# Kernel tuning notes

Hardware: AMD Instinct MI355X
Metric: run time of the kernel (lower is better)

The kernel has to match this reference:

```python
import jax, jax.numpy as jnp
import numpy as np

N_NODES = 100000
N_EDGES = 1600000
F_IN = 128
HIDDEN = 64
N_CLASSES = 32


def setup_inputs() -> dict:
    key = jax.random.key(0)
    k1, k2, k3, k4 = jax.random.split(key, 4)
    x = jax.random.normal(k1, (N_NODES, F_IN), dtype=jnp.float32)
    edge_index = jax.random.randint(k2, (2, N_EDGES), 0, N_NODES, dtype=jnp.int32)
    # Glorot-style init for the two GCNConv weight matrices
    W1 = jax.random.normal(k3, (F_IN, HIDDEN), dtype=jnp.float32) * (1.0 / np.sqrt(F_IN))
    W2 = jax.random.normal(k4, (HIDDEN, N_CLASSES), dtype=jnp.float32) * (1.0 / np.sqrt(HIDDEN))
    b1 = jnp.zeros((HIDDEN,), dtype=jnp.float32)
    b2 = jnp.zeros((N_CLASSES,), dtype=jnp.float32)
    return {"x": x, "edge_index": edge_index, "W1": W1, "b1": b1, "W2": W2, "b2": b2}


def gcn_conv(x, W, b, src, dst, num_nodes):
    # PyG GCNConv: linear transform first, then normalized neighbor aggregation.
    h = x @ W  # [N, out]
    ones = jnp.ones(src.shape, dtype=h.dtype)
    deg = jax.ops.segment_sum(ones, dst, num_segments=num_nodes)  # in-degree incl. self-loops
    d_inv_sqrt = jnp.where(deg > 0, jax.lax.rsqrt(deg), 0.0)
    norm = d_inv_sqrt[src] * d_inv_sqrt[dst]  # [E]
    msg = h[src] * norm[:, None]              # gather + scale, [E, out]
    out = jax.ops.segment_sum(msg, dst, num_segments=num_nodes)  # scatter-add
    return out + b


def reference(x, edge_index, W1, b1, W2, b2):
    n = x.shape[0]
    # add_self_loops=True (GCNConv default)
    loop = jnp.arange(n, dtype=edge_index.dtype)
    src = jnp.concatenate([edge_index[0], loop])
    dst = jnp.concatenate([edge_index[1], loop])
    h = jax.nn.relu(gcn_conv(x, W1, b1, src, dst, n))
    # F.dropout(training=self.training) is identity in eval mode
    logits = gcn_conv(h, W2, b2, src, dst, n)
    return jax.nn.log_softmax(logits, axis=1)
```

## Files before the change

### kernel.cpp

```cpp
#include <hip/hip_runtime.h>

#define F_IN 128
#define HID 64
#define CLS 32
#define BCAP 8192

typedef short v8s __attribute__((ext_vector_type(8)));
typedef float f4 __attribute__((ext_vector_type(4)));
typedef float f2 __attribute__((ext_vector_type(2)));

__device__ __forceinline__ float bflo(unsigned int w) { return __uint_as_float(w << 16); }
__device__ __forceinline__ float bfhi(unsigned int w) { return __uint_as_float(w & 0xFFFF0000u); }
__device__ __forceinline__ unsigned short f2bf(float f) {
    unsigned int u = __float_as_uint(f);
    u += 0x7FFFu + ((u >> 16) & 1u);
    return (unsigned short)(u >> 16);
}
__device__ __forceinline__ unsigned int pack2(float lo, float hi) {
    return (unsigned int)f2bf(lo) | ((unsigned int)f2bf(hi) << 16);
}
__device__ __forceinline__ unsigned char f2fp8(float v) {
    return (unsigned char)(__builtin_amdgcn_cvt_pk_fp8_f32(v, v, 0, false) & 0xFF);
}

__global__ __launch_bounds__(512) void k_init(int* __restrict__ bCursor, int nb) {
    int i = threadIdx.x;
    if (i < nb) bCursor[i] = i * BCAP;
}

__global__ __launch_bounds__(256) void k_bscatter(const int* __restrict__ src,
                                                  const int* __restrict__ dst,
                                                  int* __restrict__ bCursor,
                                                  int* __restrict__ bucketed, int E, int nb) {
    __shared__ int h[512];
    __shared__ int chunk[512];
    int tid = threadIdx.x;
    for (int i = tid; i < nb; i += 256) h[i] = 0;
    __syncthreads();

    int e0 = blockIdx.x * 2048;
    int myRec[8], myB[8], myRank[8];
#pragma unroll
    for (int k = 0; k < 8; ++k) {
        int e = e0 + k * 256 + tid;
        if (e < E) {
            int d = dst[e];
            myB[k] = d >> 8;
            myRec[k] = src[e] | ((d & 255) << 17);
            myRank[k] = atomicAdd(&h[myB[k]], 1);
        } else {
            myB[k] = -1;
        }
    }
    __syncthreads();
    for (int i = tid; i < nb; i += 256)
        chunk[i] = h[i] ? atomicAdd(&bCursor[i], h[i]) : 0;
    __syncthreads();
#pragma unroll
    for (int k = 0; k < 8; ++k) {
        if (myB[k] >= 0) bucketed[chunk[myB[k]] + myRank[k]] = myRec[k];
    }
}

__global__ __launch_bounds__(512) void k_csr(const int* __restrict__ bCursor,
                                             const int* __restrict__ bucketed,
                                             int* __restrict__ pk,
                                             float* __restrict__ dinv, int* __restrict__ csr,
                                             int n) {
    __shared__ int cnt[256];
    __shared__ int s[256];
    __shared__ int baseS[256];
    int b = blockIdx.x;
    int node0 = b << 8;
    int tid = threadIdx.x;
    if (tid < 256) cnt[tid] = 0;
    __syncthreads();
    int p0 = b * BCAP, p1 = bCursor[b];

    int rec[16], rnk[16];
#pragma unroll
    for (int k = 0; k < 16; ++k) {
        int p = p0 + tid + (k << 9);
        if (p < p1) {
            int r = bucketed[p];
            rec[k] = r;
            rnk[k] = atomicAdd(&cnt[r >> 17], 1);
        } else {
            rec[k] = -1;
        }
    }
    __syncthreads();
    int v = 0;
    if (tid < 256) { v = cnt[tid]; s[tid] = v; }
    __syncthreads();
    for (int off = 1; off < 256; off <<= 1) {
        int t = (tid >= off && tid < 256) ? s[tid - off] : 0;
        __syncthreads();
        if (tid < 256) s[tid] += t;
        __syncthreads();
    }
    if (tid < 256) {
        int myoff = p0 + s[tid] - v;
        baseS[tid] = myoff;
        int node = node0 + tid;
        if (node < n) {
            pk[node] = myoff | (v << 22);
            dinv[node] = rsqrtf((float)(v + 1));
        }
    }
    __syncthreads();
#pragma unroll
    for (int k = 0; k < 16; ++k) {
        if (rec[k] >= 0) csr[baseS[rec[k] >> 17] + rnk[k]] = rec[k] & 0x1FFFF;
    }
}

__global__ __launch_bounds__(256) void k_gemm1(const float* __restrict__ x,
                                               const float* __restrict__ W,
                                               const float* __restrict__ dinv,
                                               unsigned char* __restrict__ y, int n) {
    __shared__ unsigned short Wt[HID * 136];
    int tid = threadIdx.x;
    for (int i = tid; i < F_IN * HID; i += 256) {
        int k = i >> 6, nn = i & 63;
        Wt[nn * 136 + k] = f2bf(W[i]);
    }
    __syncthreads();

    int lane = tid & 63;
    int quad = lane >> 4, c = lane & 15;
    int nstripes = (n + 15) >> 4;
    int stripe = blockIdx.x * 4 + (tid >> 6);
    if (stripe >= nstripes) return;
    int row0 = stripe << 4;

    f4 acc[4] = {};
    union { unsigned int u[4]; v8s v; } au;

#pragma unroll
    for (int ks = 0; ks < 4; ++ks) {
        int k0 = ks * 32 + quad * 8;
        int row = row0 + c;
        if (row >= n) row = n - 1;
        const float* xp = x + (size_t)row * F_IN + k0;
        float4 lo = *(const float4*)xp;
        float4 hi = *(const float4*)(xp + 4);
        au.u[0] = pack2(lo.x, lo.y);
        au.u[1] = pack2(lo.z, lo.w);
        au.u[2] = pack2(hi.x, hi.y);
        au.u[3] = pack2(hi.z, hi.w);
        v8s a = au.v;
#pragma unroll
        for (int nt = 0; nt < 4; ++nt) {
            v8s bb = *(const v8s*)&Wt[(nt * 16 + c) * 136 + k0];
            acc[nt] = __builtin_amdgcn_mfma_f32_16x16x32_bf16(a, bb, acc[nt], 0, 0, 0);
        }
    }

#pragma unroll
    for (int reg = 0; reg < 4; ++reg) {
        int row = row0 + quad * 4 + reg;
        if (row < n) {
            float dd = dinv[row];
#pragma unroll
            for (int nt = 0; nt < 4; ++nt)
                y[(size_t)row * HID + nt * 16 + c] = f2fp8(acc[nt][reg] * dd);
        }
    }
}

__global__ __launch_bounds__(256) void k_gather64_w2(const int* __restrict__ pk,
                                                     const int* __restrict__ csr,
                                                     const unsigned char* __restrict__ xw8,
                                                     const float* __restrict__ b1,
                                                     const float* __restrict__ W2,
                                                     const float* __restrict__ dinv,
                                                     unsigned short* __restrict__ y2, int n) {
    __shared__ unsigned short Wt[CLS * 72];
    __shared__ unsigned short Hl[32 * 72];
    int tid = threadIdx.x;
    for (int i = tid; i < HID * CLS; i += 256) {
        int k = i >> 5, nn = i & 31;
        Wt[nn * 72 + k] = f2bf(W2[i]);
    }

    int g = tid >> 3;
    int l = tid & 7;
    int node = blockIdx.x * 32 + g;
    bool alive = node < n;

    if (alive) {
        unsigned int pv = (unsigned int)pk[node];
        int p0 = pv & 0x3FFFFF;
        int cntv = (int)(pv >> 22);
        int p1 = p0 + cntv;
        float dd = rsqrtf((float)(cntv + 1));
        uint2 sw = *(const uint2*)(xw8 + (size_t)node * HID + l * 8);

        f2 a0 = {0.f, 0.f}, a1 = a0, a2 = a0, a3 = a0;
        f2 c0 = a0, c1 = a0, c2 = a0, c3 = a0;
        int p = p0;
        for (; p + 3 < p1; p += 4) {
            int s0 = csr[p], s1 = csr[p + 1], s2 = csr[p + 2], s3 = csr[p + 3];
            uint2 w0 = *(const uint2*)(xw8 + (size_t)s0 * HID + l * 8);
            uint2 w1 = *(const uint2*)(xw8 + (size_t)s1 * HID + l * 8);
            uint2 w2 = *(const uint2*)(xw8 + (size_t)s2 * HID + l * 8);
            uint2 w3 = *(const uint2*)(xw8 + (size_t)s3 * HID + l * 8);
            a0 += __builtin_amdgcn_cvt_pk_f32_fp8(w0.x, false);
            a1 += __builtin_amdgcn_cvt_pk_f32_fp8(w0.x, true);
            a2 += __builtin_amdgcn_cvt_pk_f32_fp8(w0.y, false);
            a3 += __builtin_amdgcn_cvt_pk_f32_fp8(w0.y, true);
            c0 += __builtin_amdgcn_cvt_pk_f32_fp8(w1.x, false);
            c1 += __builtin_amdgcn_cvt_pk_f32_fp8(w1.x, true);
            c2 += __builtin_amdgcn_cvt_pk_f32_fp8(w1.y, false);
            c3 += __builtin_amdgcn_cvt_pk_f32_fp8(w1.y, true);
            a0 += __builtin_amdgcn_cvt_pk_f32_fp8(w2.x, false);
            a1 += __builtin_amdgcn_cvt_pk_f32_fp8(w2.x, true);
            a2 += __builtin_amdgcn_cvt_pk_f32_fp8(w2.y, false);
            a3 += __builtin_amdgcn_cvt_pk_f32_fp8(w2.y, true);
            c0 += __builtin_amdgcn_cvt_pk_f32_fp8(w3.x, false);
            c1 += __builtin_amdgcn_cvt_pk_f32_fp8(w3.x, true);
            c2 += __builtin_amdgcn_cvt_pk_f32_fp8(w3.y, false);
            c3 += __builtin_amdgcn_cvt_pk_f32_fp8(w3.y, true);
        }
        for (; p < p1; ++p) {
            int s0 = csr[p];
            uint2 w0 = *(const uint2*)(xw8 + (size_t)s0 * HID + l * 8);
            a0 += __builtin_amdgcn_cvt_pk_f32_fp8(w0.x, false);
            a1 += __builtin_amdgcn_cvt_pk_f32_fp8(w0.x, true);
            a2 += __builtin_amdgcn_cvt_pk_f32_fp8(w0.y, false);
            a3 += __builtin_amdgcn_cvt_pk_f32_fp8(w0.y, true);
        }
        a0 += c0; a1 += c1; a2 += c2; a3 += c3;
        a0 += __builtin_amdgcn_cvt_pk_f32_fp8(sw.x, false);
        a1 += __builtin_amdgcn_cvt_pk_f32_fp8(sw.x, true);
        a2 += __builtin_amdgcn_cvt_pk_f32_fp8(sw.y, false);
        a3 += __builtin_amdgcn_cvt_pk_f32_fp8(sw.y, true);

        float4 bb0 = *(const float4*)(b1 + l * 8);
        float4 bb1 = *(const float4*)(b1 + l * 8 + 4);
        float h0 = fmaxf(a0.x * dd + bb0.x, 0.f);
        float h1 = fmaxf(a0.y * dd + bb0.y, 0.f);
        float h2 = fmaxf(a1.x * dd + bb0.z, 0.f);
        float h3 = fmaxf(a1.y * dd + bb0.w, 0.f);
        float h4 = fmaxf(a2.x * dd + bb1.x, 0.f);
        float h5 = fmaxf(a2.y * dd + bb1.y, 0.f);
        float h6 = fmaxf(a3.x * dd + bb1.z, 0.f);
        float h7 = fmaxf(a3.y * dd + bb1.w, 0.f);
        uint4 hp;
        hp.x = pack2(h0, h1);
        hp.y = pack2(h2, h3);
        hp.z = pack2(h4, h5);
        hp.w = pack2(h6, h7);
        *(uint4*)&Hl[g * 72 + l * 8] = hp;
    }
    __syncthreads();

    int wv = tid >> 6;
    int t = wv & 1, nt = wv >> 1;
    int lane = tid & 63, quad = lane >> 4, c = lane & 15;
    f4 acc = {};
#pragma unroll
    for (int ks = 0; ks < 2; ++ks) {
        int k0 = ks * 32 + quad * 8;
        v8s aF = *(const v8s*)&Hl[(t * 16 + c) * 72 + k0];
        v8s bF = *(const v8s*)&Wt[(nt * 16 + c) * 72 + k0];
        acc = __builtin_amdgcn_mfma_f32_16x16x32_bf16(aF, bF, acc, 0, 0, 0);
    }
    int row0 = blockIdx.x * 32 + t * 16;
#pragma unroll
    for (int reg = 0; reg < 4; ++reg) {
        int row = row0 + quad * 4 + reg;
        if (row < n) {
            float dd2 = dinv[row];
            y2[(size_t)row * CLS + nt * 16 + c] = f2bf(acc[reg] * dd2);
        }
    }
}

__global__ __launch_bounds__(256) void k_gather32_lsm(const int* __restrict__ pk,
                                                      const int* __restrict__ csr,
                                                      const unsigned short* __restrict__ hwb,
                                                      const float* __restrict__ b,
                                                      float* __restrict__ out, int n) {
    int tid = threadIdx.x;
    int node = blockIdx.x * 64 + (tid >> 2);
    if (node >= n) return;
    int l = tid & 3;
    unsigned int pv = (unsigned int)pk[node];
    int p0 = pv & 0x3FFFFF;
    int cntv = (int)(pv >> 22);
    int p1 = p0 + cntv;
    float dd = rsqrtf((float)(cntv + 1));
    uint4 sw = *(const uint4*)(hwb + (size_t)node * CLS + l * 8);

    float A0 = 0.f, A1 = 0.f, A2 = 0.f, A3 = 0.f, A4 = 0.f, A5 = 0.f, A6 = 0.f, A7 = 0.f;
    float B0 = 0.f, B1 = 0.f, B2 = 0.f, B3 = 0.f, B4 = 0.f, B5 = 0.f, B6 = 0.f, B7 = 0.f;
    int p = p0;
    for (; p + 3 < p1; p += 4) {
        int s0 = csr[p], s1 = csr[p + 1], s2 = csr[p + 2], s3 = csr[p + 3];
        uint4 w0 = *(const uint4*)(hwb + (size_t)s0 * CLS + l * 8);
        uint4 w1 = *(const uint4*)(hwb + (size_t)s1 * CLS + l * 8);
        uint4 w2 = *(const uint4*)(hwb + (size_t)s2 * CLS + l * 8);
        uint4 w3 = *(const uint4*)(hwb + (size_t)s3 * CLS + l * 8);
        A0 += bflo(w0.x); A1 += bfhi(w0.x); A2 += bflo(w0.y); A3 += bfhi(w0.y);
        A4 += bflo(w0.z); A5 += bfhi(w0.z); A6 += bflo(w0.w); A7 += bfhi(w0.w);
        B0 += bflo(w1.x); B1 += bfhi(w1.x); B2 += bflo(w1.y); B3 += bfhi(w1.y);
        B4 += bflo(w1.z); B5 += bfhi(w1.z); B6 += bflo(w1.w); B7 += bfhi(w1.w);
        A0 += bflo(w2.x); A1 += bfhi(w2.x); A2 += bflo(w2.y); A3 += bfhi(w2.y);
        A4 += bflo(w2.z); A5 += bfhi(w2.z); A6 += bflo(w2.w); A7 += bfhi(w2.w);
        B0 += bflo(w3.x); B1 += bfhi(w3.x); B2 += bflo(w3.y); B3 += bfhi(w3.y);
        B4 += bflo(w3.z); B5 += bfhi(w3.z); B6 += bflo(w3.w); B7 += bfhi(w3.w);
    }
    for (; p < p1; ++p) {
        int s0 = csr[p];
        uint4 w0 = *(const uint4*)(hwb + (size_t)s0 * CLS + l * 8);
        A0 += bflo(w0.x); A1 += bfhi(w0.x); A2 += bflo(w0.y); A3 += bfhi(w0.y);
        A4 += bflo(w0.z); A5 += bfhi(w0.z); A6 += bflo(w0.w); A7 += bfhi(w0.w);
    }
    A0 += B0; A1 += B1; A2 += B2; A3 += B3;
    A4 += B4; A5 += B5; A6 += B6; A7 += B7;

    float4 bb0 = *(const float4*)(b + l * 8);
    float4 bb1 = *(const float4*)(b + l * 8 + 4);
    float v0 = (A0 + bflo(sw.x)) * dd + bb0.x;
    float v1 = (A1 + bfhi(sw.x)) * dd + bb0.y;
    float v2 = (A2 + bflo(sw.y)) * dd + bb0.z;
    float v3 = (A3 + bfhi(sw.y)) * dd + bb0.w;
    float v4 = (A4 + bflo(sw.z)) * dd + bb1.x;
    float v5 = (A5 + bfhi(sw.z)) * dd + bb1.y;
    float v6 = (A6 + bflo(sw.w)) * dd + bb1.z;
    float v7 = (A7 + bfhi(sw.w)) * dd + bb1.w;

    float m = fmaxf(fmaxf(fmaxf(v0, v1), fmaxf(v2, v3)), fmaxf(fmaxf(v4, v5), fmaxf(v6, v7)));
    m = fmaxf(m, __shfl_xor(m, 1));
    m = fmaxf(m, __shfl_xor(m, 2));
    float s = __expf(v0 - m) + __expf(v1 - m) + __expf(v2 - m) + __expf(v3 - m) +
              __expf(v4 - m) + __expf(v5 - m) + __expf(v6 - m) + __expf(v7 - m);
    s += __shfl_xor(s, 1);
    s += __shfl_xor(s, 2);
    float ls = m + __logf(s);
    float4 o0, o1;
    o0.x = v0 - ls; o0.y = v1 - ls; o0.z = v2 - ls; o0.w = v3 - ls;
    o1.x = v4 - ls; o1.y = v5 - ls; o1.z = v6 - ls; o1.w = v7 - ls;
    float* op = out + (size_t)node * CLS + l * 8;
    *(float4*)op = o0;
    *(float4*)(op + 4) = o1;
}

extern "C" void kernel_launch(void* const* d_in, const int* in_sizes, int n_in,
                              void* d_out, int out_size, void* d_ws, size_t ws_size,
                              hipStream_t stream) {
    const float* x  = (const float*)d_in[0];
    const int* edge = (const int*)d_in[1];
    const float* W1 = (const float*)d_in[2];
    const float* b1 = (const float*)d_in[3];
    const float* W2 = (const float*)d_in[4];
    const float* b2 = (const float*)d_in[5];
    float* out = (float*)d_out;

    int N = in_sizes[0] / F_IN;
    int E = in_sizes[1] / 2;
    const int* src = edge;
    const int* dst = edge + E;
    int NB = (N + 255) >> 8;

    float* dinv    = (float*)d_ws;
    int* pk        = (int*)(dinv + N);
    int* bCursor   = pk + N;
    int* csr       = bCursor + 512;
    int* bucketed  = csr + (size_t)NB * BCAP;
    unsigned char* bufA = (unsigned char*)(bucketed + (size_t)NB * BCAP);
    unsigned short* y2  = (unsigned short*)(bufA + (size_t)N * HID);

    k_init<<<1, 512, 0, stream>>>(bCursor, NB);
    k_bscatter<<<(E + 2047) / 2048, 256, 0, stream>>>(src, dst, bCursor, bucketed, E, NB);
    k_csr<<<NB, 512, 0, stream>>>(bCursor, bucketed, pk, dinv, csr, N);

    int nstripes16 = (N + 15) >> 4;
    int gemmBlocks = (nstripes16 + 3) / 4;

    k_gemm1<<<gemmBlocks, 256, 0, stream>>>(x, W1, dinv, bufA, N);

    k_gather64_w2<<<(N + 31) / 32, 256, 0, stream>>>(pk, csr, bufA, b1, W2, dinv, y2, N);

    k_gather32_lsm<<<(N + 63) / 64, 256, 0, stream>>>(pk, csr, y2, b2, out, N);
}
```

Before: 203.0 us.

## Fuse all GCN stages into one cooperative persistent kernel with grid syncs

Replaces the six separate launches with a single cooperative kernel. Inside it, part of the grid does the edge bucketing while the rest pulls GEMM1 jobs from an atomic work queue, so the two stages overlap. Grid-wide syncs then separate the CSR build, the layer-1 gather with the W2 transform, and the layer-2 gather with log-softmax. GEMM1 no longer depends on dinv: its output is stored unscaled and the source-side dinv is applied per neighbour during the gather. This adds an extra dinv load per edge, and grid.sync overhead plus the lower per-CU occupancy cap can offset the saved launches. The bf16 packing also switches to the v_cvt_pk_bf16_f32 instruction.

```diff
diff --git a/kernel.cpp b/kernel.cpp
--- a/kernel.cpp
+++ b/kernel.cpp
@@ -1,4 +1,7 @@
 #include <hip/hip_runtime.h>
+#include <hip/hip_cooperative_groups.h>
+
+namespace cg = cooperative_groups;
 
 #define F_IN 128
 #define HID 64
@@ -17,335 +20,324 @@
     return (unsigned short)(u >> 16);
 }
 __device__ __forceinline__ unsigned int pack2(float lo, float hi) {
-    return (unsigned int)f2bf(lo) | ((unsigned int)f2bf(hi) << 16);
+    unsigned int r;
+    asm("v_cvt_pk_bf16_f32 %0, %1, %2" : "=v"(r) : "v"(lo), "v"(hi));
+    return r;
 }
 __device__ __forceinline__ unsigned char f2fp8(float v) {
     return (unsigned char)(__builtin_amdgcn_cvt_pk_fp8_f32(v, v, 0, false) & 0xFF);
 }
 
-__global__ __launch_bounds__(512) void k_init(int* __restrict__ bCursor, int nb) {
-    int i = threadIdx.x;
-    if (i < nb) bCursor[i] = i * BCAP;
-}
-
-__global__ __launch_bounds__(256) void k_bscatter(const int* __restrict__ src,
-                                                  const int* __restrict__ dst,
-                                                  int* __restrict__ bCursor,
-                                                  int* __restrict__ bucketed, int E, int nb) {
-    __shared__ int h[512];
-    __shared__ int chunk[512];
-    int tid = threadIdx.x;
-    for (int i = tid; i < nb; i += 256) h[i] = 0;
-    __syncthreads();
-
-    int e0 = blockIdx.x * 2048;
-    int myRec[8], myB[8], myRank[8];
-#pragma unroll
-    for (int k = 0; k < 8; ++k) {
-        int e = e0 + k * 256 + tid;
-        if (e < E) {
-            int d = dst[e];
-            myB[k] = d >> 8;
-            myRec[k] = src[e] | ((d & 255) << 17);
-            myRank[k] = atomicAdd(&h[myB[k]], 1);
-        } else {
-            myB[k] = -1;
-        }
-    }
-    __syncthreads();
-    for (int i = tid; i < nb; i += 256)
-        chunk[i] = h[i] ? atomicAdd(&bCursor[i], h[i]) : 0;
-    __syncthreads();
-#pragma unroll
-    for (int k = 0; k < 8; ++k) {
-        if (myB[k] >= 0) bucketed[chunk[myB[k]] + myRank[k]] = myRec[k];
-    }
-}
-
-__global__ __launch_bounds__(512) void k_csr(const int* __restrict__ bCursor,
-                                             const int* __restrict__ bucketed,
-                                             int* __restrict__ pk,
-                                             float* __restrict__ dinv, int* __restrict__ csr,
-                                             int n) {
-    __shared__ int cnt[256];
-    __shared__ int s[256];
-    __shared__ int baseS[256];
-    int b = blockIdx.x;
-    int node0 = b << 8;
-    int tid = threadIdx.x;
-    if (tid < 256) cnt[tid] = 0;
-    __syncthreads();
-    int p0 = b * BCAP, p1 = bCursor[b];
-
-    int rec[16], rnk[16];
-#pragma unroll
-    for (int k = 0; k < 16; ++k) {
-        int p = p0 + tid + (k << 9);
-        if (p < p1) {
-            int r = bucketed[p];
-            rec[k] = r;
-            rnk[k] = atomicAdd(&cnt[r >> 17], 1);
-        } else {
-            rec[k] = -1;
-        }
-    }
-    __syncthreads();
-    int v = 0;
-    if (tid < 256) { v = cnt[tid]; s[tid] = v; }
-    __syncthreads();
-    for (int off = 1; off < 256; off <<= 1) {
-        int t = (tid >= off && tid < 256) ? s[tid - off] : 0;
-        __syncthreads();
-        if (tid < 256) s[tid] += t;
-        __syncthreads();
-    }
-    if (tid < 256) {
-        int myoff = p0 + s[tid] - v;
-        baseS[tid] = myoff;
-        int node = node0 + tid;
-        if (node < n) {
-            pk[node] = myoff | (v << 22);
-            dinv[node] = rsqrtf((float)(v + 1));
-        }
-    }
-    __syncthreads();
-#pragma unroll
-    for (int k = 0; k < 16; ++k) {
-        if (rec[k] >= 0) csr[baseS[rec[k] >> 17] + rnk[k]] = rec[k] & 0x1FFFF;
-    }
-}
-
-__global__ __launch_bounds__(256) void k_gemm1(const float* __restrict__ x,
-                                               const float* __restrict__ W,
-                                               const float* __restrict__ dinv,
-                                               unsigned char* __restrict__ y, int n) {
-    __shared__ unsigned short Wt[HID * 136];
-    int tid = threadIdx.x;
-    for (int i = tid; i < F_IN * HID; i += 256) {
-        int k = i >> 6, nn = i & 63;
-        Wt[nn * 136 + k] = f2bf(W[i]);
-    }
-    __syncthreads();
-
-    int lane = tid & 63;
-    int quad = lane >> 4, c = lane & 15;
-    int nstripes = (n + 15) >> 4;
-    int stripe = blockIdx.x * 4 + (tid >> 6);
-    if (stripe >= nstripes) return;
-    int row0 = stripe << 4;
-
-    f4 acc[4] = {};
-    union { unsigned int u[4]; v8s v; } au;
-
-#pragma unroll
-    for (int ks = 0; ks < 4; ++ks) {
-        int k0 = ks * 32 + quad * 8;
-        int row = row0 + c;
-        if (row >= n) row = n - 1;
-        const float* xp = x + (size_t)row * F_IN + k0;
-        float4 lo = *(const float4*)xp;
-        float4 hi = *(const float4*)(xp + 4);
-        au.u[0] = pack2(lo.x, lo.y);
-        au.u[1] = pack2(lo.z, lo.w);
-        au.u[2] = pack2(hi.x, hi.y);
-        au.u[3] = pack2(hi.z, hi.w);
-        v8s a = au.v;
-#pragma unroll
-        for (int nt = 0; nt < 4; ++nt) {
-            v8s bb = *(const v8s*)&Wt[(nt * 16 + c) * 136 + k0];
-            acc[nt] = __builtin_amdgcn_mfma_f32_16x16x32_bf16(a, bb, acc[nt], 0, 0, 0);
-        }
-    }
-
-#pragma unroll
-    for (int reg = 0; reg < 4; ++reg) {
-        int row = row0 + quad * 4 + reg;
-        if (row < n) {
-            float dd = dinv[row];
-#pragma unroll
-            for (int nt = 0; nt < 4; ++nt)
-                y[(size_t)row * HID + nt * 16 + c] = f2fp8(acc[nt][reg] * dd);
-        }
-    }
-}
-
-__global__ __launch_bounds__(256) void k_gather64_w2(const int* __restrict__ pk,
-                                                     const int* __restrict__ csr,
-                                                     const unsigned char* __restrict__ xw8,
-                                                     const float* __restrict__ b1,
-                                                     const float* __restrict__ W2,
-                                                     const float* __restrict__ dinv,
-                                                     unsigned short* __restrict__ y2, int n) {
-    __shared__ unsigned short Wt[CLS * 72];
-    __shared__ unsigned short Hl[32 * 72];
-    int tid = threadIdx.x;
+struct GP {
+    const float* x; const int* src; const int* dst;
+    const float* W1; const float* b1; const float* W2; const float* b2;
+    float* out;
+    float* dinv; int* pk; int* bC; int* qctr; int* csr; int* bucketed;
+    unsigned char* bufA; unsigned short* y2;
+    int N, E, NB, split;
+};
+
+union SU {
+    struct { int h[512]; int chunk[512]; } sc;
+    struct { int cnt[256]; int s[256]; int cur[256]; } cs;
+    unsigned short w1[HID * 136];
+    struct { unsigned short Wt[CLS * 72]; unsigned short Hl[32 * 72]; } g;
+};
+
+__global__ __launch_bounds__(256, 4) void k_fused(GP p) {
+    __shared__ SU S;
+    __shared__ int jslot;
+    cg::grid_group grid = cg::this_grid();
+    const int tid = threadIdx.x;
+    const int bid = blockIdx.x;
+    const int GD = gridDim.x;
+    const int lane = tid & 63;
+
+    if (bid < p.split) {
+        int nchunks = (p.E + 2047) >> 11;
+        for (int ch = bid; ch < nchunks; ch += p.split) {
+            __syncthreads();
+            for (int i = tid; i < p.NB; i += 256) S.sc.h[i] = 0;
+            __syncthreads();
+            int e0 = ch << 11;
+            int myRec[8], myB[8], myRank[8];
+#pragma unroll
+            for (int k = 0; k < 8; ++k) {
+                int e = e0 + k * 256 + tid;
+                if (e < p.E) {
+                    int d = p.dst[e];
+                    myB[k] = d >> 8;
+                    myRec[k] = p.src[e] | ((d & 255) << 17);
+                    myRank[k] = atomicAdd(&S.sc.h[myB[k]], 1);
+                } else {
+                    myB[k] = -1;
+                }
+            }
+            __syncthreads();
+            for (int i = tid; i < p.NB; i += 256)
+                S.sc.chunk[i] = S.sc.h[i] ? (i * BCAP + atomicAdd(&p.bC[i], S.sc.h[i])) : 0;
+            __syncthreads();
+#pragma unroll
+            for (int k = 0; k < 8; ++k)
+                if (myB[k] >= 0) p.bucketed[S.sc.chunk[myB[k]] + myRank[k]] = myRec[k];
+        }
+        __syncthreads();
+    }
+    {
+        for (int i = tid; i < F_IN * HID; i += 256) {
+            int k = i >> 6, nn = i & 63;
+            S.w1[nn * 136 + k] = f2bf(p.W1[i]);
+        }
+        int nstripes = (p.N + 15) >> 4;
+        int jobs = (nstripes + 3) >> 2;
+        int quad = lane >> 4, c = lane & 15;
+        while (true) {
+            __syncthreads();
+            if (tid == 0) jslot = atomicAdd(p.qctr, 1);
+            __syncthreads();
+            int job = jslot;
+            if (job >= jobs) break;
+            int stripe = job * 4 + (tid >> 6);
+            if (stripe < nstripes) {
+                int row0 = stripe << 4;
+                f4 acc[4] = {};
+                union { unsigned int u[4]; v8s v; } au;
+#pragma unroll
+                for (int ks = 0; ks < 4; ++ks) {
+                    int k0 = ks * 32 + quad * 8;
+                    int row = row0 + c;
+                    if (row >= p.N) row = p.N - 1;
+                    const float* xp = p.x + (size_t)row * F_IN + k0;
+                    float4 lo = *(const float4*)xp;
+                    float4 hi = *(const float4*)(xp + 4);
+                    au.u[0] = pack2(lo.x, lo.y);
+                    au.u[1] = pack2(lo.z, lo.w);
+                    au.u[2] = pack2(hi.x, hi.y);
+                    au.u[3] = pack2(hi.z, hi.w);
+                    v8s a = au.v;
+#pragma unroll
+                    for (int nt = 0; nt < 4; ++nt) {
+                        v8s bb = *(const v8s*)&S.w1[(nt * 16 + c) * 136 + k0];
+                        acc[nt] = __builtin_amdgcn_mfma_f32_16x16x32_bf16(a, bb, acc[nt], 0, 0, 0);
+                    }
+                }
+#pragma unroll
+                for (int reg = 0; reg < 4; ++reg) {
+                    int row = row0 + quad * 4 + reg;
+                    if (row < p.N) {
+#pragma unroll
+                        for (int nt = 0; nt < 4; ++nt)
+                            p.bufA[(size_t)row * HID + nt * 16 + c] = f2fp8(acc[nt][reg]);
+                    }
+                }
+            }
+        }
+    }
+    grid.sync();
+
+    for (int b = bid; b < p.NB; b += GD) {
+        __syncthreads();
+        S.cs.cnt[tid] = 0;
+        __syncthreads();
+        int p0 = b * BCAP, p1 = p0 + p.bC[b];
+        for (int q = p0 + tid; q < p1; q += 256) atomicAdd(&S.cs.cnt[p.bucketed[q] >> 17], 1);
+        __syncthreads();
+        int v = S.cs.cnt[tid];
+        S.cs.s[tid] = v;
+        __syncthreads();
+        for (int off = 1; off < 256; off <<= 1) {
+            int t = (tid >= off) ? S.cs.s[tid - off] : 0;
+            __syncthreads();
+            S.cs.s[tid] += t;
+            __syncthreads();
+        }
+        int myoff = p0 + S.cs.s[tid] - v;
+        S.cs.cur[tid] = myoff;
+        int node = (b << 8) + tid;
+        if (node < p.N) {
+            p.pk[node] = myoff | (v << 22);
+            p.dinv[node] = rsqrtf((float)(v + 1));
+        }
+        __syncthreads();
+        for (int q = p0 + tid; q < p1; q += 256) {
+            int r = p.bucketed[q];
+            int w = atomicAdd(&S.cs.cur[r >> 17], 1);
+            p.csr[w] = r & 0x1FFFF;
+        }
+    }
+    grid.sync();
+
     for (int i = tid; i < HID * CLS; i += 256) {
         int k = i >> 5, nn = i & 31;
-        Wt[nn * 72 + k] = f2bf(W2[i]);
-    }
-
-    int g = tid >> 3;
-    int l = tid & 7;
-    int node = blockIdx.x * 32 + g;
-    bool alive = node < n;
-
-    if (alive) {
-        unsigned int pv = (unsigned int)pk[node];
-        int p0 = pv & 0x3FFFFF;
-        int cntv = (int)(pv >> 22);
-        int p1 = p0 + cntv;
-        float dd = rsqrtf((float)(cntv + 1));
-        uint2 sw = *(const uint2*)(xw8 + (size_t)node * HID + l * 8);
-
-        f2 a0 = {0.f, 0.f}, a1 = a0, a2 = a0, a3 = a0;
-        f2 c0 = a0, c1 = a0, c2 = a0, c3 = a0;
-        int p = p0;
-        for (; p + 3 < p1; p += 4) {
-            int s0 = csr[p], s1 = csr[p + 1], s2 = csr[p + 2], s3 = csr[p + 3];
-            uint2 w0 = *(const uint2*)(xw8 + (size_t)s0 * HID + l * 8);
-            uint2 w1 = *(const uint2*)(xw8 + (size_t)s1 * HID + l * 8);
-            uint2 w2 = *(const uint2*)(xw8 + (size_t)s2 * HID + l * 8);
-            uint2 w3 = *(const uint2*)(xw8 + (size_t)s3 * HID + l * 8);
-            a0 += __builtin_amdgcn_cvt_pk_f32_fp8(w0.x, false);
-            a1 += __builtin_amdgcn_cvt_pk_f32_fp8(w0.x, true);
-            a2 += __builtin_amdgcn_cvt_pk_f32_fp8(w0.y, false);
-            a3 += __builtin_amdgcn_cvt_pk_f32_fp8(w0.y, true);
-            c0 += __builtin_amdgcn_cvt_pk_f32_fp8(w1.x, false);
-            c1 += __builtin_amdgcn_cvt_pk_f32_fp8(w1.x, true);
-            c2 += __builtin_amdgcn_cvt_pk_f32_fp8(w1.y, false);
-            c3 += __builtin_amdgcn_cvt_pk_f32_fp8(w1.y, true);
-            a0 += __builtin_amdgcn_cvt_pk_f32_fp8(w2.x, false);
-            a1 += __builtin_amdgcn_cvt_pk_f32_fp8(w2.x, true);
-            a2 += __builtin_amdgcn_cvt_pk_f32_fp8(w2.y, false);
-            a3 += __builtin_amdgcn_cvt_pk_f32_fp8(w2.y, true);
-            c0 += __builtin_amdgcn_cvt_pk_f32_fp8(w3.x, false);
-            c1 += __builtin_amdgcn_cvt_pk_f32_fp8(w3.x, true);
-            c2 += __builtin_amdgcn_cvt_pk_f32_fp8(w3.y, false);
-            c3 += __builtin_amdgcn_cvt_pk_f32_fp8(w3.y, true);
-        }
-        for (; p < p1; ++p) {
-            int s0 = csr[p];
-            uint2 w0 = *(const uint2*)(xw8 + (size_t)s0 * HID + l * 8);
-            a0 += __builtin_amdgcn_cvt_pk_f32_fp8(w0.x, false);
-            a1 += __builtin_amdgcn_cvt_pk_f32_fp8(w0.x, true);
-            a2 += __builtin_amdgcn_cvt_pk_f32_fp8(w0.y, false);
-            a3 += __builtin_amdgcn_cvt_pk_f32_fp8(w0.y, true);
-        }
-        a0 += c0; a1 += c1; a2 += c2; a3 += c3;
-        a0 += __builtin_amdgcn_cvt_pk_f32_fp8(sw.x, false);
-        a1 += __builtin_amdgcn_cvt_pk_f32_fp8(sw.x, true);
-        a2 += __builtin_amdgcn_cvt_pk_f32_fp8(sw.y, false);
-        a3 += __builtin_amdgcn_cvt_pk_f32_fp8(sw.y, true);
-
-        float4 bb0 = *(const float4*)(b1 + l * 8);
-        float4 bb1 = *(const float4*)(b1 + l * 8 + 4);
-        float h0 = fmaxf(a0.x * dd + bb0.x, 0.f);
-        float h1 = fmaxf(a0.y * dd + bb0.y, 0.f);
-        float h2 = fmaxf(a1.x * dd + bb0.z, 0.f);
-        float h3 = fmaxf(a1.y * dd + bb0.w, 0.f);
-        float h4 = fmaxf(a2.x * dd + bb1.x, 0.f);
-        float h5 = fmaxf(a2.y * dd + bb1.y, 0.f);
-        float h6 = fmaxf(a3.x * dd + bb1.z, 0.f);
-        float h7 = fmaxf(a3.y * dd + bb1.w, 0.f);
-        uint4 hp;
-        hp.x = pack2(h0, h1);
-        hp.y = pack2(h2, h3);
-        hp.z = pack2(h4, h5);
-        hp.w = pack2(h6, h7);
-        *(uint4*)&Hl[g * 72 + l * 8] = hp;
-    }
-    __syncthreads();
-
-    int wv = tid >> 6;
-    int t = wv & 1, nt = wv >> 1;
-    int lane = tid & 63, quad = lane >> 4, c = lane & 15;
-    f4 acc = {};
-#pragma unroll
-    for (int ks = 0; ks < 2; ++ks) {
-        int k0 = ks * 32 + quad * 8;
-        v8s aF = *(const v8s*)&Hl[(t * 16 + c) * 72 + k0];
-        v8s bF = *(const v8s*)&Wt[(nt * 16 + c) * 72 + k0];
-        acc = __builtin_amdgcn_mfma_f32_16x16x32_bf16(aF, bF, acc, 0, 0, 0);
-    }
-    int row0 = blockIdx.x * 32 + t * 16;
-#pragma unroll
-    for (int reg = 0; reg < 4; ++reg) {
-        int row = row0 + quad * 4 + reg;
-        if (row < n) {
-            float dd2 = dinv[row];
-            y2[(size_t)row * CLS + nt * 16 + c] = f2bf(acc[reg] * dd2);
-        }
-    }
-}
-
-__global__ __launch_bounds__(256) void k_gather32_lsm(const int* __restrict__ pk,
-                                                      const int* __restrict__ csr,
-                                                      const unsigned short* __restrict__ hwb,
-                                                      const float* __restrict__ b,
-                                                      float* __restrict__ out, int n) {
-    int tid = threadIdx.x;
-    int node = blockIdx.x * 64 + (tid >> 2);
-    if (node >= n) return;
-    int l = tid & 3;
-    unsigned int pv = (unsigned int)pk[node];
-    int p0 = pv & 0x3FFFFF;
-    int cntv = (int)(pv >> 22);
-    int p1 = p0 + cntv;
-    float dd = rsqrtf((float)(cntv + 1));
-    uint4 sw = *(const uint4*)(hwb + (size_t)node * CLS + l * 8);
-
-    float A0 = 0.f, A1 = 0.f, A2 = 0.f, A3 = 0.f, A4 = 0.f, A5 = 0.f, A6 = 0.f, A7 = 0.f;
-    float B0 = 0.f, B1 = 0.f, B2 = 0.f, B3 = 0.f, B4 = 0.f, B5 = 0.f, B6 = 0.f, B7 = 0.f;
-    int p = p0;
-    for (; p + 3 < p1; p += 4) {
-        int s0 = csr[p], s1 = csr[p + 1], s2 = csr[p + 2], s3 = csr[p + 3];
-        uint4 w0 = *(const uint4*)(hwb + (size_t)s0 * CLS + l * 8);
-        uint4 w1 = *(const uint4*)(hwb + (size_t)s1 * CLS + l * 8);
-        uint4 w2 = *(const uint4*)(hwb + (size_t)s2 * CLS + l * 8);
-        uint4 w3 = *(const uint4*)(hwb + (size_t)s3 * CLS + l * 8);
-        A0 += bflo(w0.x); A1 += bfhi(w0.x); A2 += bflo(w0.y); A3 += bfhi(w0.y);
-        A4 += bflo(w0.z); A5 += bfhi(w0.z); A6 += bflo(w0.w); A7 += bfhi(w0.w);
-        B0 += bflo(w1.x); B1 += bfhi(w1.x); B2 += bflo(w1.y); B3 += bfhi(w1.y);
-        B4 += bflo(w1.z); B5 += bfhi(w1.z); B6 += bflo(w1.w); B7 += bfhi(w1.w);
-        A0 += bflo(w2.x); A1 += bfhi(w2.x); A2 += bflo(w2.y); A3 += bfhi(w2.y);
-        A4 += bflo(w2.z); A5 += bfhi(w2.z); A6 += bflo(w2.w); A7 += bfhi(w2.w);
-        B0 += bflo(w3.x); B1 += bfhi(w3.x); B2 += bflo(w3.y); B3 += bfhi(w3.y);
-        B4 += bflo(w3.z); B5 += bfhi(w3.z); B6 += bflo(w3.w); B7 += bfhi(w3.w);
-    }
-    for (; p < p1; ++p) {
-        int s0 = csr[p];
-        uint4 w0 = *(const uint4*)(hwb + (size_t)s0 * CLS + l * 8);
-        A0 += bflo(w0.x); A1 += bfhi(w0.x); A2 += bflo(w0.y); A3 += bfhi(w0.y);
-        A4 += bflo(w0.z); A5 += bfhi(w0.z); A6 += bflo(w0.w); A7 += bfhi(w0.w);
-    }
-    A0 += B0; A1 += B1; A2 += B2; A3 += B3;
-    A4 += B4; A5 += B5; A6 += B6; A7 += B7;
-
-    float4 bb0 = *(const float4*)(b + l * 8);
-    float4 bb1 = *(const float4*)(b + l * 8 + 4);
-    float v0 = (A0 + bflo(sw.x)) * dd + bb0.x;
-    float v1 = (A1 + bfhi(sw.x)) * dd + bb0.y;
-    float v2 = (A2 + bflo(sw.y)) * dd + bb0.z;
-    float v3 = (A3 + bfhi(sw.y)) * dd + bb0.w;
-    float v4 = (A4 + bflo(sw.z)) * dd + bb1.x;
-    float v5 = (A5 + bfhi(sw.z)) * dd + bb1.y;
-    float v6 = (A6 + bflo(sw.w)) * dd + bb1.z;
-    float v7 = (A7 + bfhi(sw.w)) * dd + bb1.w;
-
-    float m = fmaxf(fmaxf(fmaxf(v0, v1), fmaxf(v2, v3)), fmaxf(fmaxf(v4, v5), fmaxf(v6, v7)));
-    m = fmaxf(m, __shfl_xor(m, 1));
-    m = fmaxf(m, __shfl_xor(m, 2));
-    float s = __expf(v0 - m) + __expf(v1 - m) + __expf(v2 - m) + __expf(v3 - m) +
-              __expf(v4 - m) + __expf(v5 - m) + __expf(v6 - m) + __expf(v7 - m);
-    s += __shfl_xor(s, 1);
-    s += __shfl_xor(s, 2);
-    float ls = m + __logf(s);
-    float4 o0, o1;
-    o0.x = v0 - ls; o0.y = v1 - ls; o0.z = v2 - ls; o0.w = v3 - ls;
-    o1.x = v4 - ls; o1.y = v5 - ls; o1.z = v6 - ls; o1.w = v7 - ls;
-    float* op = out + (size_t)node * CLS + l * 8;
-    *(float4*)op = o0;
-    *(float4*)(op + 4) = o1;
+        S.g.Wt[nn * 72 + k] = f2bf(p.W2[i]);
+    }
+    {
+        int g = tid >> 3, l = tid & 7;
+        int wv = tid >> 6;
+        int t = wv & 1, nt = wv >> 1;
+        int quad = lane >> 4, c = lane & 15;
+        int jobs3 = (p.N + 31) >> 5;
+        for (int job = bid; job < jobs3; job += GD) {
+            __syncthreads();
+            int node = (job << 5) + g;
+            if (node < p.N) {
+                unsigned int pv = (unsigned int)p.pk[node];
+                int p0 = pv & 0x3FFFFF;
+                int cntv = (int)(pv >> 22);
+                int p1 = p0 + cntv;
+                float dd = rsqrtf((float)(cntv + 1));
+                uint2 sw = *(const uint2*)(p.bufA + (size_t)node * HID + l * 8);
+
+                f2 a0 = {0.f, 0.f}, a1 = a0, a2 = a0, a3 = a0;
+                f2 c0 = a0, c1 = a0, c2 = a0, c3 = a0;
+                int q = p0;
+                for (; q + 3 < p1; q += 4) {
+                    int s0 = p.csr[q], s1 = p.csr[q + 1], s2 = p.csr[q + 2], s3 = p.csr[q + 3];
+                    float d0 = p.dinv[s0], d1 = p.dinv[s1], d2 = p.dinv[s2], d3 = p.dinv[s3];
+                    uint2 w0 = *(const uint2*)(p.bufA + (size_t)s0 * HID + l * 8);
+                    uint2 w1 = *(const uint2*)(p.bufA + (size_t)s1 * HID + l * 8);
+                    uint2 w2 = *(const uint2*)(p.bufA + (size_t)s2 * HID + l * 8);
+                    uint2 w3 = *(const uint2*)(p.bufA + (size_t)s3 * HID + l * 8);
+                    f2 D0 = {d0, d0}, D1 = {d1, d1}, D2 = {d2, d2}, D3 = {d3, d3};
+                    a0 += __builtin_amdgcn_cvt_pk_f32_fp8(w0.x, false) * D0;
+                    a1 += __builtin_amdgcn_cvt_pk_f32_fp8(w0.x, true) * D0;
+                    a2 += __builtin_amdgcn_cvt_pk_f32_fp8(w0.y, false) * D0;
+                    a3 += __builtin_amdgcn_cvt_pk_f32_fp8(w0.y, true) * D0;
+                    c0 += __builtin_amdgcn_cvt_pk_f32_fp8(w1.x, false) * D1;
+                    c1 += __builtin_amdgcn_cvt_pk_f32_fp8(w1.x, true) * D1;
+                    c2 += __builtin_amdgcn_cvt_pk_f32_fp8(w1.y, false) * D1;
+                    c3 += __builtin_amdgcn_cvt_pk_f32_fp8(w1.y, true) * D1;
+                    a0 += __builtin_amdgcn_cvt_pk_f32_fp8(w2.x, false) * D2;
+                    a1 += __builtin_amdgcn_cvt_pk_f32_fp8(w2.x, true) * D2;
+                    a2 += __builtin_amdgcn_cvt_pk_f32_fp8(w2.y, false) * D2;
+                    a3 += __builtin_amdgcn_cvt_pk_f32_fp8(w2.y, true) * D2;
+                    c0 += __builtin_amdgcn_cvt_pk_f32_fp8(w3.x, false) * D3;
+                    c1 += __builtin_amdgcn_cvt_pk_f32_fp8(w3.x, true) * D3;
+                    c2 += __builtin_amdgcn_cvt_pk_f32_fp8(w3.y, false) * D3;
+                    c3 += __builtin_amdgcn_cvt_pk_f32_fp8(w3.y, true) * D3;
+                }
+                for (; q < p1; ++q) {
+                    int s0 = p.csr[q];
+                    float d0 = p.dinv[s0];
+                    uint2 w0 = *(const uint2*)(p.bufA + (size_t)s0 * HID + l * 8);
+                    f2 D0 = {d0, d0};
+                    a0 += __builtin_amdgcn_cvt_pk_f32_fp8(w0.x, false) * D0;
+                    a1 += __builtin_amdgcn_cvt_pk_f32_fp8(w0.x, true) * D0;
+                    a2 += __builtin_amdgcn_cvt_pk_f32_fp8(w0.y, false) * D0;
+                    a3 += __builtin_amdgcn_cvt_pk_f32_fp8(w0.y, true) * D0;
+                }
+                a0 += c0; a1 += c1; a2 += c2; a3 += c3;
+                f2 DS = {dd, dd};
+                a0 += __builtin_amdgcn_cvt_pk_f32_fp8(sw.x, false) * DS;
+                a1 += __builtin_amdgcn_cvt_pk_f32_fp8(sw.x, true) * DS;
+                a2 += __builtin_amdgcn_cvt_pk_f32_fp8(sw.y, false) * DS;
+                a3 += __builtin_amdgcn_cvt_pk_f32_fp8(sw.y, true) * DS;
+
+                float4 bb0 = *(const float4*)(p.b1 + l * 8);
+                float4 bb1 = *(const float4*)(p.b1 + l * 8 + 4);
+                float h0 = fmaxf(a0.x * dd + bb0.x, 0.f);
+                float h1 = fmaxf(a0.y * dd + bb0.y, 0.f);
+                float h2 = fmaxf(a1.x * dd + bb0.z, 0.f);
+                float h3 = fmaxf(a1.y * dd + bb0.w, 0.f);
+                float h4 = fmaxf(a2.x * dd + bb1.x, 0.f);
+                float h5 = fmaxf(a2.y * dd + bb1.y, 0.f);
+                float h6 = fmaxf(a3.x * dd + bb1.z, 0.f);
+                float h7 = fmaxf(a3.y * dd + bb1.w, 0.f);
+                uint4 hp;
+                hp.x = pack2(h0, h1);
+                hp.y = pack2(h2, h3);
+                hp.z = pack2(h4, h5);
+                hp.w = pack2(h6, h7);
+                *(uint4*)&S.g.Hl[g * 72 + l * 8] = hp;
+            }
+            __syncthreads();
+            f4 acc = {};
+#pragma unroll
+            for (int ks = 0; ks < 2; ++ks) {
+                int k0 = ks * 32 + quad * 8;
+                v8s aF = *(const v8s*)&S.g.Hl[(t * 16 + c) * 72 + k0];
+                v8s bF = *(const v8s*)&S.g.Wt[(nt * 16 + c) * 72 + k0];
+                acc = __builtin_amdgcn_mfma_f32_16x16x32_bf16(aF, bF, acc, 0, 0, 0);
+            }
+            int row0 = (job << 5) + t * 16;
+#pragma unroll
+            for (int reg = 0; reg < 4; ++reg) {
+                int row = row0 + quad * 4 + reg;
+                if (row < p.N)
+                    p.y2[(size_t)row * CLS + nt * 16 + c] = f2bf(acc[reg] * p.dinv[row]);
+            }
+        }
+    }
+    grid.sync();
+
+    {
+        int jobs4 = (p.N + 63) >> 6;
+        int l = tid & 3;
+        for (int job = bid; job < jobs4; job += GD) {
+            int node = (job << 6) + (tid >> 2);
+            if (node >= p.N) continue;
+            unsigned int pv = (unsigned int)p.pk[node];
+            int p0 = pv & 0x3FFFFF;
+            int cntv = (int)(pv >> 22);
+            int p1 = p0 + cntv;
+            float dd = rsqrtf((float)(cntv + 1));
+            uint4 sw = *(const uint4*)(p.y2 + (size_t)node * CLS + l * 8);
+
+            float A0 = 0.f, A1 = 0.f, A2 = 0.f, A3 = 0.f, A4 = 0.f, A5 = 0.f, A6 = 0.f, A7 = 0.f;
+            float B0 = 0.f, B1 = 0.f, B2 = 0.f, B3 = 0.f, B4 = 0.f, B5 = 0.f, B6 = 0.f, B7 = 0.f;
+            int q = p0;
+            for (; q + 3 < p1; q += 4) {
+                int s0 = p.csr[q], s1 = p.csr[q + 1], s2 = p.csr[q + 2], s3 = p.csr[q + 3];
+                uint4 w0 = *(const uint4*)(p.y2 + (size_t)s0 * CLS + l * 8);
+                uint4 w1 = *(const uint4*)(p.y2 + (size_t)s1 * CLS + l * 8);
+                uint4 w2 = *(const uint4*)(p.y2 + (size_t)s2 * CLS + l * 8);
+                uint4 w3 = *(const uint4*)(p.y2 + (size_t)s3 * CLS + l * 8);
+                A0 += bflo(w0.x); A1 += bfhi(w0.x); A2 += bflo(w0.y); A3 += bfhi(w0.y);
+                A4 += bflo(w0.z); A5 += bfhi(w0.z); A6 += bflo(w0.w); A7 += bfhi(w0.w);
+                B0 += bflo(w1.x); B1 += bfhi(w1.x); B2 += bflo(w1.y); B3 += bfhi(w1.y);
+                B4 += bflo(w1.z); B5 += bfhi(w1.z); B6 += bflo(w1.w); B7 += bfhi(w1.w);
+                A0 += bflo(w2.x); A1 += bfhi(w2.x); A2 += bflo(w2.y); A3 += bfhi(w2.y);
+                A4 += bflo(w2.z); A5 += bfhi(w2.z); A6 += bflo(w2.w); A7 += bfhi(w2.w);
+                B0 += bflo(w3.x); B1 += bfhi(w3.x); B2 += bflo(w3.y); B3 += bfhi(w3.y);
+                B4 += bflo(w3.z); B5 += bfhi(w3.z); B6 += bflo(w3.w); B7 += bfhi(w3.w);
+            }
+            for (; q < p1; ++q) {
+                int s0 = p.csr[q];
+                uint4 w0 = *(const uint4*)(p.y2 + (size_t)s0 * CLS + l * 8);
+                A0 += bflo(w0.x); A1 += bfhi(w0.x); A2 += bflo(w0.y); A3 += bfhi(w0.y);
+                A4 += bflo(w0.z); A5 += bfhi(w0.z); A6 += bflo(w0.w); A7 += bfhi(w0.w);
+            }
+            A0 += B0; A1 += B1; A2 += B2; A3 += B3;
+            A4 += B4; A5 += B5; A6 += B6; A7 += B7;
+
+            float4 bb0 = *(const float4*)(p.b2 + l * 8);
+            float4 bb1 = *(const float4*)(p.b2 + l * 8 + 4);
+            float v0 = (A0 + bflo(sw.x)) * dd + bb0.x;
+            float v1 = (A1 + bfhi(sw.x)) * dd + bb0.y;
+            float v2 = (A2 + bflo(sw.y)) * dd + bb0.z;
+            float v3 = (A3 + bfhi(sw.y)) * dd + bb0.w;
+            float v4 = (A4 + bflo(sw.z)) * dd + bb1.x;
+            float v5 = (A5 + bfhi(sw.z)) * dd + bb1.y;
+            float v6 = (A6 + bflo(sw.w)) * dd + bb1.z;
+            float v7 = (A7 + bfhi(sw.w)) * dd + bb1.w;
+
+            float m = fmaxf(fmaxf(fmaxf(v0, v1), fmaxf(v2, v3)),
+                            fmaxf(fmaxf(v4, v5), fmaxf(v6, v7)));
+            m = fmaxf(m, __shfl_xor(m, 1));
+            m = fmaxf(m, __shfl_xor(m, 2));
+            float s = __expf(v0 - m) + __expf(v1 - m) + __expf(v2 - m) + __expf(v3 - m) +
+                      __expf(v4 - m) + __expf(v5 - m) + __expf(v6 - m) + __expf(v7 - m);
+            s += __shfl_xor(s, 1);
+            s += __shfl_xor(s, 2);
+            float ls = m + __logf(s);
+            float4 o0, o1;
+            o0.x = v0 - ls; o0.y = v1 - ls; o0.z = v2 - ls; o0.w = v3 - ls;
+            o1.x = v4 - ls; o1.y = v5 - ls; o1.z = v6 - ls; o1.w = v7 - ls;
+            float* op = p.out + (size_t)node * CLS + l * 8;
+            *(float4*)op = o0;
+            *(float4*)(op + 4) = o1;
+        }
+    }
 }
 
 extern "C" void kernel_launch(void* const* d_in, const int* in_sizes, int n_in,
@@ -367,22 +359,42 @@
 
     float* dinv    = (float*)d_ws;
     int* pk        = (int*)(dinv + N);
-    int* bCursor   = pk + N;
-    int* csr       = bCursor + 512;
+    int* bC        = pk + N;
+    int* qctr      = bC + NB;
+    int* csr       = bC + 512;
     int* bucketed  = csr + (size_t)NB * BCAP;
     unsigned char* bufA = (unsigned char*)(bucketed + (size_t)NB * BCAP);
     unsigned short* y2  = (unsigned short*)(bufA + (size_t)N * HID);
 
-    k_init<<<1, 512, 0, stream>>>(bCursor, NB);
-    k_bscatter<<<(E + 2047) / 2048, 256, 0, stream>>>(src, dst, bCursor, bucketed, E, NB);
-    k_csr<<<NB, 512, 0, stream>>>(bCursor, bucketed, pk, dinv, csr, N);
-
-    int nstripes16 = (N + 15) >> 4;
-    int gemmBlocks = (nstripes16 + 3) / 4;
-
-    k_gemm1<<<gemmBlocks, 256, 0, stream>>>(x, W1, dinv, bufA, N);
-
-    k_gather64_w2<<<(N + 31) / 32, 256, 0, stream>>>(pk, csr, bufA, b1, W2, dinv, y2, N);
-
-    k_gather32_lsm<<<(N + 63) / 64, 256, 0, stream>>>(pk, csr, y2, b2, out, N);
+    hipMemsetAsync(bC, 0, (size_t)(NB + 1) * sizeof(int), stream);
+
+    static int blocksPerCU = 0;
+    static int numCU = 0;
+    if (blocksPerCU == 0) {
+        int r = 0;
+        hipOccupancyMaxActiveBlocksPerMultiprocessor(&r, k_fused, 256, 0);
+        blocksPerCU = (r > 0) ? r : 4;
+        hipDeviceProp_t prop;
+        int dev = 0;
+        hipGetDevice(&dev);
+        if (hipGetDeviceProperties(&prop, dev) == hipSuccess && prop.multiProcessorCount > 0)
+            numCU = prop.multiProcessorCount;
+        else
+            numCU = 256;
+    }
+    int GRID = blocksPerCU * numCU;
+    if (GRID > 2048) GRID = 2048;
+    if (GRID < 64) GRID = 64;
+
+    GP hp;
+    hp.x = x; hp.src = src; hp.dst = dst;
+    hp.W1 = W1; hp.b1 = b1; hp.W2 = W2; hp.b2 = b2;
+    hp.out = out;
+    hp.dinv = dinv; hp.pk = pk; hp.bC = bC; hp.qctr = qctr;
+    hp.csr = csr; hp.bucketed = bucketed; hp.bufA = bufA; hp.y2 = y2;
+    hp.N = N; hp.E = E; hp.NB = NB;
+    hp.split = (GRID * 3) / 8;
+
+    void* args[] = { &hp };
+    hipLaunchCooperativeKernel(k_fused, dim3(GRID), dim3(256), args, 0, stream);
 }
```

Measured after the change: 525.9 us. +159.1%, slower.
